# Kernel tuning notes

Measured on AMD Instinct MI355X. Metric: run time of the kernel, lower is better.

## Reference

```python
import jax, jax.numpy as jnp
import numpy as np

B, S, D, H, W = 2, 2048, 1024, 16, 16  # batch, seq, embed, heads, window
HD = D // H
DFF = 4 * D
EPS = 1e-5


def _ln(x, g, b):
    m = jnp.mean(x, axis=-1, keepdims=True)
    v = jnp.mean(jnp.square(x - m), axis=-1, keepdims=True)
    return (x - m) * jax.lax.rsqrt(v + EPS) * g + b


def setup_inputs() -> dict:
    key = jax.random.key(0)
    ks = jax.random.split(key, 12)
    s = 0.02
    return {
        "x": jax.random.normal(ks[0], (B, S, D), jnp.float32),
        "ln1_g": jnp.ones((D,), jnp.float32),
        "ln1_b": jnp.zeros((D,), jnp.float32),
        "in_proj_w": jax.random.normal(ks[1], (3 * D, D), jnp.float32) * s,
        "in_proj_b": jnp.zeros((3 * D,), jnp.float32),
        "out_proj_w": jax.random.normal(ks[2], (D, D), jnp.float32) * s,
        "out_proj_b": jnp.zeros((D,), jnp.float32),
        "ln2_g": jnp.ones((D,), jnp.float32),
        "ln2_b": jnp.zeros((D,), jnp.float32),
        "mlp_w1": jax.random.normal(ks[3], (DFF, D), jnp.float32) * s,
        "mlp_b1": jnp.zeros((DFF,), jnp.float32),
        "mlp_w2": jax.random.normal(ks[4], (D, DFF), jnp.float32) * s,
        "mlp_b2": jnp.zeros((D,), jnp.float32),
    }


def reference(x, ln1_g, ln1_b, in_proj_w, in_proj_b, out_proj_w, out_proj_b,
              ln2_g, ln2_b, mlp_w1, mlp_b1, mlp_w2, mlp_b2):
    h = _ln(x, ln1_g, ln1_b)
    qkv = h @ in_proj_w.T + in_proj_b  # [B,S,3D]
    q, k, v = jnp.split(qkv, 3, axis=-1)
    q = q.reshape(B, S, H, HD)
    k = k.reshape(B, S, H, HD)
    v = v.reshape(B, S, H, HD)
    scores = jnp.einsum("bqhd,bkhd->bhqk", q, k) / jnp.sqrt(jnp.float32(HD))
    idx = jnp.arange(S)
    dlt = idx[:, None] - idx[None, :]
    allowed = (dlt >= 0) & (dlt < W)  # causal sliding window, width W
    scores = jnp.where(allowed, scores, -jnp.inf)
    attn = jax.nn.softmax(scores, axis=-1)
    o = jnp.einsum("bhqk,bkhd->bqhd", attn, v).reshape(B, S, D)
    o = o @ out_proj_w.T + out_proj_b
    x = x + o  # residual 1
    xn = _ln(x, ln2_g, ln2_b)
    mlp = jax.nn.gelu(xn @ mlp_w1.T + mlp_b1) @ mlp_w2.T + mlp_b2
    return x + mlp
```

## Files before the change

kernel.cpp:

```cpp
#include <hip/hip_runtime.h>
#include <hip/hip_bf16.h>
#include <cmath>

typedef __bf16 bf16;
typedef __bf16 bf16x4 __attribute__((ext_vector_type(4)));
typedef __bf16 bf16x8 __attribute__((ext_vector_type(8)));
typedef float f32x4 __attribute__((ext_vector_type(4)));

#define BB 2
#define SS 2048
#define DD 1024
#define HH 16
#define WW 16
#define HDD 64
#define DFFD 4096
#define NTOK (BB*SS)

__device__ __forceinline__ float gelu_f(float x) {
    const float k = 1.5957691216057308f;
    float u = k * (x + 0.044715f * x * x * x);
    return x / (1.0f + __expf(-u));
}

__device__ __forceinline__ void glds16(const bf16* g, const bf16* l) {
    __builtin_amdgcn_global_load_lds(
        (const __attribute__((address_space(1))) void*)(uintptr_t)(const void*)g,
        (__attribute__((address_space(3))) void*)(unsigned)(uintptr_t)(const void*)l,
        16, 0, 0);
}

__global__ __launch_bounds__(256) void conv2ln_kernel(
    const float* __restrict__ s0, bf16* __restrict__ d0, int n0,
    const float* __restrict__ s1, bf16* __restrict__ d1, int n1, int ncb,
    const float* __restrict__ xin, const float* __restrict__ g,
    const float* __restrict__ b, bf16* __restrict__ lnout)
{
    const int t = threadIdx.x;
    if ((int)blockIdx.x < ncb) {
        int i = blockIdx.x * 256 + t;
        const float* src; bf16* dst; int idx;
        if (i < n0) { src = s0; dst = d0; idx = i; }
        else        { idx = i - n0; if (idx >= n1) return; src = s1; dst = d1; }
        f32x4 a = *(const f32x4*)(src + (size_t)idx * 8);
        f32x4 c = *(const f32x4*)(src + (size_t)idx * 8 + 4);
        bf16x8 v;
#pragma unroll
        for (int j = 0; j < 4; j++) { v[j] = (bf16)a[j]; v[4 + j] = (bf16)c[j]; }
        *(bf16x8*)(dst + (size_t)idx * 8) = v;
        return;
    }
    const int row = blockIdx.x - ncb;
    f32x4 v = *(const f32x4*)(xin + (size_t)row * DD + t * 4);
    float s  = v[0] + v[1] + v[2] + v[3];
    float s2 = v[0]*v[0] + v[1]*v[1] + v[2]*v[2] + v[3]*v[3];
#pragma unroll
    for (int off = 32; off >= 1; off >>= 1) {
        s  += __shfl_xor(s,  off, 64);
        s2 += __shfl_xor(s2, off, 64);
    }
    __shared__ float red[8];
    const int wave = t >> 6;
    if ((t & 63) == 0) { red[wave] = s; red[4 + wave] = s2; }
    __syncthreads();
    float ts  = red[0] + red[1] + red[2] + red[3];
    float ts2 = red[4] + red[5] + red[6] + red[7];
    float mean = ts * (1.0f / DD);
    float var  = ts2 * (1.0f / DD) - mean * mean;
    float rstd = rsqrtf(var + 1e-5f);
    f32x4 gv = *(const f32x4*)(g + t * 4);
    f32x4 bv = *(const f32x4*)(b + t * 4);
    bf16x4 o;
#pragma unroll
    for (int i = 0; i < 4; i++) o[i] = (bf16)((v[i] - mean) * rstd * gv[i] + bv[i]);
    *(bf16x4*)(lnout + (size_t)row * DD + t * 4) = o;
}

template<int TM, int ACT, int RESID, int OUTF32>
__global__ __launch_bounds__(256) void gemm_glds(
    const bf16* __restrict__ A, const bf16* __restrict__ Bw,
    const float* __restrict__ bias,
    const float* resid, void* __restrict__ Cout, int N, int K)
{
    constexpr int MI = 4;
    constexpr int NJ = (TM == 128) ? 4 : 2;
    __shared__ __align__(16) bf16 As[4 * TM * 32];
    __shared__ __align__(16) bf16 Bs[4 * 128 * 32];
    const int t = threadIdx.x;
    const int nbxy = gridDim.x * gridDim.y;
    const int bid  = blockIdx.y * gridDim.x + blockIdx.x;
    const int cpx  = nbxy >> 3;
    const int swz  = (bid & 7) * cpx + (bid >> 3);
    const int m0 = (swz / gridDim.x) * TM;
    const int n0 = (swz % gridDim.x) * 128;
    const int lane = t & 63, w = t >> 6;
    const int wm = (TM == 128) ? (w & 1) * 64 : 0;
    const int wn = (TM == 128) ? (w >> 1) * 64 : w * 32;
    const int quad = lane >> 4, l16 = lane & 15;
    const int srow = t >> 2;
    const int qsw  = (t & 3) ^ ((srow >> 1) & 3);

    const bf16* Ag = A  + (size_t)(m0 + srow) * K + qsw * 8;
    const bf16* Bg = Bw + (size_t)(n0 + srow) * K + qsw * 8;

    int k_lo = 0, k_hi = K;
    if (RESID == 3) {
        const int ks = K / gridDim.z;
        k_lo = blockIdx.z * ks;
        k_hi = k_lo + ks;
    }

    auto stage = [&](int buf, int k0) {
        const bf16* AsW = As + buf * (TM * 32) + w * 512;
        const bf16* BsW = Bs + buf * (128 * 32) + w * 512;
        glds16(Ag + k0, AsW);
        if (TM == 128) glds16(Ag + (size_t)64 * K + k0, AsW + 2048);
        glds16(Bg + k0, BsW);
        glds16(Bg + (size_t)64 * K + k0, BsW + 2048);
    };

    const f32x4 zero = {0.f, 0.f, 0.f, 0.f};
    f32x4 acc[MI][NJ];
#pragma unroll
    for (int i = 0; i < MI; i++)
#pragma unroll
        for (int j = 0; j < NJ; j++) acc[i][j] = zero;

    const int nsteps = (k_hi - k_lo) >> 5;
    stage(0, k_lo);
    if (nsteps > 1) stage(1, k_lo + 32);
    if (nsteps > 2) stage(2, k_lo + 64);

    const int rsl = (quad ^ ((l16 >> 1) & 3)) * 8;
    for (int step = 0; step < nsteps; ++step) {
        if (step < nsteps - 2) {
            if (TM == 128) asm volatile("s_waitcnt vmcnt(8)" ::: "memory");
            else           asm volatile("s_waitcnt vmcnt(6)" ::: "memory");
        } else if (step == nsteps - 2) {
            if (TM == 128) asm volatile("s_waitcnt vmcnt(4)" ::: "memory");
            else           asm volatile("s_waitcnt vmcnt(3)" ::: "memory");
        } else {
            asm volatile("s_waitcnt vmcnt(0)" ::: "memory");
        }
        __builtin_amdgcn_s_barrier();
        if (step + 3 < nsteps) stage((step + 3) & 3, k_lo + ((step + 3) << 5));
        const bf16* Ab = As + (step & 3) * (TM * 32);
        const bf16* Bb = Bs + (step & 3) * (128 * 32);
        bf16x8 af[MI], bfr[NJ];
#pragma unroll
        for (int i = 0; i < MI; i++)
            af[i] = *(const bf16x8*)(Ab + (wm + i * 16 + l16) * 32 + rsl);
#pragma unroll
        for (int j = 0; j < NJ; j++)
            bfr[j] = *(const bf16x8*)(Bb + (wn + j * 16 + l16) * 32 + rsl);
#pragma unroll
        for (int i = 0; i < MI; i++)
#pragma unroll
            for (int j = 0; j < NJ; j++)
                acc[i][j] = __builtin_amdgcn_mfma_f32_16x16x32_bf16(af[i], bfr[j], acc[i][j], 0, 0, 0);
    }

#pragma unroll
    for (int i = 0; i < MI; i++) {
#pragma unroll
        for (int j = 0; j < NJ; j++) {
            int col = n0 + wn + j * 16 + l16;
            float bv = bias[col];
            if (RESID == 3 && blockIdx.z != 0) bv = 0.0f;
#pragma unroll
            for (int r = 0; r < 4; r++) {
                int row = m0 + wm + i * 16 + quad * 4 + r;
                float val = acc[i][j][r] + bv;
                if (ACT == 1) val = gelu_f(val);
                size_t idx = (size_t)row * N + col;
                if (RESID == 2) val += resid[idx];
                if (RESID == 3) {
                    unsafeAtomicAdd(&((float*)Cout)[idx], val);
                } else if (OUTF32) {
                    ((float*)Cout)[idx] = val;
                } else {
                    ((bf16*)Cout)[idx] = (bf16)val;
                }
            }
        }
    }
}

__global__ __launch_bounds__(256) void attn_kernel(
    const bf16* __restrict__ qkv, bf16* __restrict__ o)
{
    __shared__ __align__(16) bf16 Vlds[4][32 * 64];
    __shared__ __align__(16) bf16 Plds[4][16 * 32];
    const int t = threadIdx.x;
    const int w = t >> 6, lane = t & 63;
    const int quad = lane >> 4, l16 = lane & 15;
    const int gw = blockIdx.x * 4 + w;
    const int qb = gw & 127;
    const int h  = (gw >> 7) & (HH - 1);
    const int b  = gw >> 11;
    const int q0 = qb << 4;
    const size_t rs = 3 * DD;
    const bf16* Qb = qkv + (size_t)b * SS * rs + h * HDD;
    const bf16* Kb = Qb + DD;
    const bf16* Vb = Qb + 2 * DD;
    bf16* Vw = Vlds[w];
    bf16* Pw = Plds[w];

    {
        const int sub = lane >> 3;
        const int dc  = (lane & 7) * 8;
#pragma unroll
        for (int c = 0; c < 4; c++) {
            int key = q0 - 16 + c * 8 + sub;
            if (key < 0) key = 0;
            glds16(Vb + (size_t)key * rs + dc, Vw + c * 512);
        }
    }

    const int qrow = q0 + l16;
    int kr0 = q0 - 16 + l16; if (kr0 < 0) kr0 = 0;
    bf16x8 qf0  = *(const bf16x8*)(Qb + (size_t)qrow * rs + quad * 8);
    bf16x8 qf1  = *(const bf16x8*)(Qb + (size_t)qrow * rs + 32 + quad * 8);
    bf16x8 kf0a = *(const bf16x8*)(Kb + (size_t)kr0  * rs + quad * 8);
    bf16x8 kf0b = *(const bf16x8*)(Kb + (size_t)kr0  * rs + 32 + quad * 8);
    bf16x8 kf1a = *(const bf16x8*)(Kb + (size_t)qrow * rs + quad * 8);
    bf16x8 kf1b = *(const bf16x8*)(Kb + (size_t)qrow * rs + 32 + quad * 8);

    const f32x4 zero = {0.f, 0.f, 0.f, 0.f};
    f32x4 acc0 = __builtin_amdgcn_mfma_f32_16x16x32_bf16(qf0, kf0a, zero, 0, 0, 0);
    acc0 = __builtin_amdgcn_mfma_f32_16x16x32_bf16(qf1, kf0b, acc0, 0, 0, 0);
    f32x4 acc1 = __builtin_amdgcn_mfma_f32_16x16x32_bf16(qf0, kf1a, zero, 0, 0, 0);
    acc1 = __builtin_amdgcn_mfma_f32_16x16x32_bf16(qf1, kf1b, acc1, 0, 0, 0);

    float rl[4];
#pragma unroll
    for (int r = 0; r < 4; r++) {
        const int row = quad * 4 + r;
        float s0 = (l16 > row && q0 - 16 + l16 >= 0) ? acc0[r] * 0.125f : -1e30f;
        float s1 = (l16 <= row)                      ? acc1[r] * 0.125f : -1e30f;
        float m = fmaxf(s0, s1);
        m = fmaxf(m, __shfl_xor(m, 1, 64));
        m = fmaxf(m, __shfl_xor(m, 2, 64));
        m = fmaxf(m, __shfl_xor(m, 4, 64));
        m = fmaxf(m, __shfl_xor(m, 8, 64));
        float e0 = __expf(s0 - m), e1 = __expf(s1 - m);
        float sum = e0 + e1;
        sum += __shfl_xor(sum, 1, 64);
        sum += __shfl_xor(sum, 2, 64);
        sum += __shfl_xor(sum, 4, 64);
        sum += __shfl_xor(sum, 8, 64);
        rl[r] = 1.0f / sum;
        Pw[row * 32 + l16]      = (bf16)e0;
        Pw[row * 32 + 16 + l16] = (bf16)e1;
    }

    asm volatile("s_waitcnt vmcnt(0)" ::: "memory");
    bf16x8 pf = *(const bf16x8*)(Pw + l16 * 32 + quad * 8);
#pragma unroll
    for (int dt = 0; dt < 4; dt++) {
        bf16x8 vf;
#pragma unroll
        for (int jj = 0; jj < 8; jj++)
            vf[jj] = Vw[(quad * 8 + jj) * 64 + dt * 16 + l16];
        f32x4 ov = __builtin_amdgcn_mfma_f32_16x16x32_bf16(pf, vf, zero, 0, 0, 0);
#pragma unroll
        for (int r = 0; r < 4; r++) {
            const int row = quad * 4 + r;
            o[(size_t)(b * SS + q0 + row) * DD + h * HDD + dt * 16 + l16] =
                (bf16)(ov[r] * rl[r]);
        }
    }
}

extern "C" void kernel_launch(void* const* d_in, const int* in_sizes, int n_in,
                              void* d_out, int out_size, void* d_ws, size_t ws_size,
                              hipStream_t stream)
{
    (void)in_sizes; (void)n_in; (void)out_size; (void)ws_size;
    const float* x    = (const float*)d_in[0];
    const float* ln1g = (const float*)d_in[1];
    const float* ln1b = (const float*)d_in[2];
    const float* Wqkv = (const float*)d_in[3];
    const float* bqkv = (const float*)d_in[4];
    const float* Wout = (const float*)d_in[5];
    const float* bout = (const float*)d_in[6];
    const float* ln2g = (const float*)d_in[7];
    const float* ln2b = (const float*)d_in[8];
    const float* W1   = (const float*)d_in[9];
    const float* b1   = (const float*)d_in[10];
    const float* W2   = (const float*)d_in[11];
    const float* b2   = (const float*)d_in[12];

    const size_t MB = (size_t)1 << 20;
    char* ws = (char*)d_ws;
    bf16* wqkv_bf = (bf16*)(ws);
    bf16* wout_bf = (bf16*)(ws + 6 * MB);
    bf16* w1_bf   = (bf16*)(ws);
    bf16* w2_bf   = (bf16*)(ws + 8 * MB);
    bf16* qkv     = (bf16*)(ws + 16 * MB);
    bf16* h1      = (bf16*)(ws + 16 * MB);
    bf16* hbuf    = (bf16*)(ws + 48 * MB);
    float* x1     = (float*)d_out;

    const dim3 blk(256);

    {
        const int n0 = 3 * DD * DD / 8, n1 = DD * DD / 8;
        const int ncb = (n0 + n1) / 256;
        conv2ln_kernel<<<ncb + NTOK, blk, 0, stream>>>(
            Wqkv, wqkv_bf, n0, Wout, wout_bf, n1, ncb, x, ln1g, ln1b, hbuf);
    }
    gemm_glds<128, 0, 0, 0><<<dim3(24, 32), blk, 0, stream>>>(
        hbuf, wqkv_bf, bqkv, nullptr, qkv, 3 * DD, DD);
    attn_kernel<<<BB * HH * (SS / 16) / 4, blk, 0, stream>>>(qkv, hbuf);
    gemm_glds<64, 0, 2, 1><<<dim3(8, 64), blk, 0, stream>>>(
        hbuf, wout_bf, bout, x, x1, DD, DD);

    {
        const int n0 = DFFD * DD / 8, n1 = DFFD * DD / 8;
        const int ncb = (n0 + n1) / 256;
        conv2ln_kernel<<<ncb + NTOK, blk, 0, stream>>>(
            W1, w1_bf, n0, W2, w2_bf, n1, ncb, x1, ln2g, ln2b, hbuf);
    }
    gemm_glds<128, 1, 0, 0><<<dim3(32, 32), blk, 0, stream>>>(
        hbuf, w1_bf, b1, nullptr, h1, DFFD, DD);
    gemm_glds<128, 0, 3, 1><<<dim3(8, 32, 2), blk, 0, stream>>>(
        h1, w2_bf, b2, nullptr, x1, DD, DFFD);
}
```

Baseline: 298.4 us.

## Use 256-row tiles for MLP up-projection and triple-buffer GEMM staging

Adds a TM=256 GEMM variant (8x4 MFMA fragments per wave) and uses it for the first MLP GEMM, halving the M-direction grid so each block reuses B tiles across more rows. The shared-memory pipeline drops from four buffers with three-ahead prefetch to three buffers with two-ahead prefetch, and the kernel gets a launch_bounds occupancy hint of two blocks per CU. Larger tiles raise register pressure and reduce the block count, and the shallower prefetch may expose more load latency.

```diff
diff --git a/kernel.cpp b/kernel.cpp
--- a/kernel.cpp
+++ b/kernel.cpp
@@ -76,15 +76,16 @@
 }
 
 template<int TM, int ACT, int RESID, int OUTF32>
-__global__ __launch_bounds__(256) void gemm_glds(
+__global__ __launch_bounds__(256, 2) void gemm_glds(
     const bf16* __restrict__ A, const bf16* __restrict__ Bw,
     const float* __restrict__ bias,
     const float* resid, void* __restrict__ Cout, int N, int K)
 {
-    constexpr int MI = 4;
-    constexpr int NJ = (TM == 128) ? 4 : 2;
-    __shared__ __align__(16) bf16 As[4 * TM * 32];
-    __shared__ __align__(16) bf16 Bs[4 * 128 * 32];
+    constexpr int MI  = (TM == 256) ? 8 : 4;
+    constexpr int NJ  = (TM == 64) ? 2 : 4;
+    constexpr int ACH = TM / 64;
+    __shared__ __align__(16) bf16 As[3 * TM * 32];
+    __shared__ __align__(16) bf16 Bs[3 * 128 * 32];
     const int t = threadIdx.x;
     const int nbxy = gridDim.x * gridDim.y;
     const int bid  = blockIdx.y * gridDim.x + blockIdx.x;
@@ -93,8 +94,8 @@
     const int m0 = (swz / gridDim.x) * TM;
     const int n0 = (swz % gridDim.x) * 128;
     const int lane = t & 63, w = t >> 6;
-    const int wm = (TM == 128) ? (w & 1) * 64 : 0;
-    const int wn = (TM == 128) ? (w >> 1) * 64 : w * 32;
+    const int wm = (TM == 256) ? (w & 1) * 128 : (TM == 128) ? (w & 1) * 64 : 0;
+    const int wn = (TM == 64) ? w * 32 : (w >> 1) * 64;
     const int quad = lane >> 4, l16 = lane & 15;
     const int srow = t >> 2;
     const int qsw  = (t & 3) ^ ((srow >> 1) & 3);
@@ -112,8 +113,9 @@
     auto stage = [&](int buf, int k0) {
         const bf16* AsW = As + buf * (TM * 32) + w * 512;
         const bf16* BsW = Bs + buf * (128 * 32) + w * 512;
-        glds16(Ag + k0, AsW);
-        if (TM == 128) glds16(Ag + (size_t)64 * K + k0, AsW + 2048);
+#pragma unroll
+        for (int c = 0; c < ACH; c++)
+            glds16(Ag + (size_t)(c * 64) * K + k0, AsW + c * 2048);
         glds16(Bg + k0, BsW);
         glds16(Bg + (size_t)64 * K + k0, BsW + 2048);
     };
@@ -128,23 +130,21 @@
     const int nsteps = (k_hi - k_lo) >> 5;
     stage(0, k_lo);
     if (nsteps > 1) stage(1, k_lo + 32);
-    if (nsteps > 2) stage(2, k_lo + 64);
 
     const int rsl = (quad ^ ((l16 >> 1) & 3)) * 8;
+    int cur = 0, nxt2 = 2;
     for (int step = 0; step < nsteps; ++step) {
-        if (step < nsteps - 2) {
-            if (TM == 128) asm volatile("s_waitcnt vmcnt(8)" ::: "memory");
-            else           asm volatile("s_waitcnt vmcnt(6)" ::: "memory");
-        } else if (step == nsteps - 2) {
-            if (TM == 128) asm volatile("s_waitcnt vmcnt(4)" ::: "memory");
-            else           asm volatile("s_waitcnt vmcnt(3)" ::: "memory");
+        if (step < nsteps - 1) {
+            if constexpr (TM == 256)      asm volatile("s_waitcnt vmcnt(6)" ::: "memory");
+            else if constexpr (TM == 128) asm volatile("s_waitcnt vmcnt(4)" ::: "memory");
+            else                          asm volatile("s_waitcnt vmcnt(3)" ::: "memory");
         } else {
             asm volatile("s_waitcnt vmcnt(0)" ::: "memory");
         }
         __builtin_amdgcn_s_barrier();
-        if (step + 3 < nsteps) stage((step + 3) & 3, k_lo + ((step + 3) << 5));
-        const bf16* Ab = As + (step & 3) * (TM * 32);
-        const bf16* Bb = Bs + (step & 3) * (128 * 32);
+        if (step + 2 < nsteps) stage(nxt2, k_lo + ((step + 2) << 5));
+        const bf16* Ab = As + cur * (TM * 32);
+        const bf16* Bb = Bs + cur * (128 * 32);
         bf16x8 af[MI], bfr[NJ];
 #pragma unroll
         for (int i = 0; i < MI; i++)
@@ -157,6 +157,8 @@
 #pragma unroll
             for (int j = 0; j < NJ; j++)
                 acc[i][j] = __builtin_amdgcn_mfma_f32_16x16x32_bf16(af[i], bfr[j], acc[i][j], 0, 0, 0);
+        cur  = (cur  + 1 == 3) ? 0 : cur  + 1;
+        nxt2 = (nxt2 + 1 == 3) ? 0 : nxt2 + 1;
     }
 
 #pragma unroll
@@ -321,7 +323,7 @@
         conv2ln_kernel<<<ncb + NTOK, blk, 0, stream>>>(
             W1, w1_bf, n0, W2, w2_bf, n1, ncb, x1, ln2g, ln2b, hbuf);
     }
-    gemm_glds<128, 1, 0, 0><<<dim3(32, 32), blk, 0, stream>>>(
+    gemm_glds<256, 1, 0, 0><<<dim3(32, 16), blk, 0, stream>>>(
         hbuf, w1_bf, b1, nullptr, h1, DFFD, DD);
     gemm_glds<128, 0, 3, 1><<<dim3(8, 32, 2), blk, 0, stream>>>(
         h1, w2_bf, b2, nullptr, x1, DD, DFFD);
```

Measured after the change: 288.1 us. 3.5% less time.
